# Optimization experiments

Measured on AMD Instinct MI355X. Metric: run time of the kernel, lower is better.

Reference implementation:

```python
import jax, jax.numpy as jnp
import numpy as np

N_NODES = 50000
N_RAND_EDGES = 800000
NEG_SLOPE = 0.2


def setup_inputs() -> dict:
    key = jax.random.key(0)
    ks = jax.random.split(key, 10)
    src_r = jax.random.randint(ks[0], (N_RAND_EDGES,), 0, N_NODES, dtype=jnp.int32)
    dst_r = jax.random.randint(ks[1], (N_RAND_EDGES,), 0, N_NODES, dtype=jnp.int32)
    loops = jnp.arange(N_NODES, dtype=jnp.int32)
    src = jnp.concatenate([src_r, loops])  # [E] with self-loops -> no empty softmax segment
    dst = jnp.concatenate([dst_r, loops])
    return {
        "x": jax.random.normal(ks[2], (N_NODES, 256), dtype=jnp.float32),
        "src": src,
        "dst": dst,
        "W0": jax.random.normal(ks[3], (256, 4 * 64), dtype=jnp.float32) * 0.05,
        "al0": jax.random.normal(ks[4], (4, 64), dtype=jnp.float32) * 0.05,
        "ar0": jax.random.normal(ks[5], (4, 64), dtype=jnp.float32) * 0.05,
        "W1": jax.random.normal(ks[6], (256, 1 * 32), dtype=jnp.float32) * 0.05,
        "al1": jax.random.normal(ks[7], (1, 32), dtype=jnp.float32) * 0.05,
        "ar1": jax.random.normal(ks[8], (1, 32), dtype=jnp.float32) * 0.05,
        "Wres": jax.random.normal(ks[9], (256, 32), dtype=jnp.float32) * 0.05,
    }


def gat_conv(x, src, dst, W, al, ar, Wres, activation):
    """DGL-style GATConv. x: [N, F]; W: [F, H*D]; al/ar: [H, D]."""
    N = x.shape[0]
    H, D = al.shape
    feat = (x @ W).reshape(N, H, D)                       # [N,H,D]
    el = jnp.sum(feat * al, axis=-1)                      # [N,H]
    er = jnp.sum(feat * ar, axis=-1)                      # [N,H]
    e = jax.nn.leaky_relu(el[src] + er[dst], NEG_SLOPE)   # [E,H]
    # edge softmax over incoming edges of each dst node
    emax = jax.ops.segment_max(e, dst, num_segments=N)    # [N,H]
    ex = jnp.exp(e - emax[dst])
    denom = jax.ops.segment_sum(ex, dst, num_segments=N)  # [N,H]
    alpha = ex / denom[dst]                               # [E,H]
    msg = feat[src] * alpha[:, :, None]                   # [E,H,D]
    out = jax.ops.segment_sum(msg, dst, num_segments=N)   # [N,H,D]
    if Wres is not None:
        out = out + (x @ Wres).reshape(N, -1, D)          # residual (broadcast over heads)
    if activation is not None:
        out = activation(out)
    return out


def reference(x, src, dst, W0, al0, ar0, W1, al1, ar1, Wres):
    N = x.shape[0]
    h = gat_conv(x, src, dst, W0, al0, ar0, None, jax.nn.elu)  # [N,4,64]
    h = h.reshape(N, -1)                                       # flatten(1) -> [N,256]
    out = gat_conv(h, src, dst, W1, al1, ar1, Wres, None)      # [N,1,32]
    logits = out.mean(axis=1)                                  # [N,32]
    return logits
```

## Files before the change

### kernel.cpp

```cpp
#include <hip/hip_runtime.h>
#include <math.h>

#define NEG_SLOPE 0.2f

typedef __attribute__((ext_vector_type(8))) short short8;
typedef __attribute__((ext_vector_type(4))) float f32x4;
typedef unsigned int uintx2 __attribute__((ext_vector_type(2)));
typedef unsigned int uintx4 __attribute__((ext_vector_type(4)));

__device__ __forceinline__ float leaky(float x) { return x > 0.f ? x : NEG_SLOPE * x; }
__device__ __forceinline__ unsigned enc(float f) {
    unsigned u = __float_as_uint(f);
    return (u & 0x80000000u) ? ~u : (u | 0x80000000u);
}
__device__ __forceinline__ float dec(unsigned e) {
    return (e & 0x80000000u) ? __uint_as_float(e ^ 0x80000000u) : __uint_as_float(~e);
}
__device__ __forceinline__ unsigned bf16u(float f) {
    unsigned u = __float_as_uint(f);
    return (u + 0x7fffu + ((u >> 16) & 1u)) >> 16;
}
__device__ __forceinline__ float blo(unsigned u) { return __uint_as_float(u << 16); }
__device__ __forceinline__ float bhi(unsigned u) { return __uint_as_float(u & 0xffff0000u); }

__global__ __launch_bounds__(256) void prep_kernel(const float* __restrict__ W0,
                                                   unsigned short* __restrict__ W0P,
                                                   const float* __restrict__ W1,
                                                   const float* __restrict__ Wres,
                                                   unsigned short* __restrict__ Bt1,
                                                   const int* __restrict__ dst,
                                                   int* __restrict__ deg, int E) {
    int b = blockIdx.x, tid = threadIdx.x;
    if (b < 256) {
        int n = b, k = tid;
        W0P[(k >> 5) * 8192 + n * 32 + (k & 31)] = (unsigned short)bf16u(W0[k * 256 + n]);
    } else if (b < 320) {
        int n = b - 256, k = tid;
        float v = (n < 32) ? W1[k * 32 + n] : Wres[k * 32 + (n - 32)];
        Bt1[n * 256 + k] = (unsigned short)bf16u(v);
    } else {
        int e = (b - 320) * 256 + tid;
        if (e < E) atomicAdd(&deg[dst[e]], 1);
    }
}

__global__ __launch_bounds__(256) void gemm0_all(const float* __restrict__ x,
                                                 const unsigned short* __restrict__ W0P,
                                                 unsigned short* __restrict__ featS,
                                                 float* __restrict__ el0, float* __restrict__ er0,
                                                 const float* __restrict__ al,
                                                 const float* __restrict__ ar,
                                                 unsigned* __restrict__ gmax, int M) {
    __shared__ unsigned short As[64 * 40];
    __shared__ unsigned short Bs[256 * 40];
    __shared__ __align__(16) unsigned short tile[64 * 72];
    __shared__ float sEl[4][64], sEr[4][64];
    const int K = 256;
    int tid = threadIdx.x, lane = tid & 63, wv = tid >> 6;
    int m0 = blockIdx.x * 64;
    int wm = (wv >> 1) * 32, wn = (wv & 1) * 32;
    f32x4 acc[4][2][2] = {};
    int arow = tid >> 2, apart = tid & 3;
    bool avalid = (m0 + arow) < M;
    const float* Ap = x + (size_t)min(m0 + arow, M - 1) * K + apart * 8;

    for (int k0 = 0; k0 < K; k0 += 32) {
        float4 a0 = avalid ? *(const float4*)(Ap + k0) : make_float4(0.f, 0.f, 0.f, 0.f);
        float4 a1 = avalid ? *(const float4*)(Ap + k0 + 4) : make_float4(0.f, 0.f, 0.f, 0.f);
        uint4 ap;
        ap.x = bf16u(a0.x) | (bf16u(a0.y) << 16);
        ap.y = bf16u(a0.z) | (bf16u(a0.w) << 16);
        ap.z = bf16u(a1.x) | (bf16u(a1.y) << 16);
        ap.w = bf16u(a1.z) | (bf16u(a1.w) << 16);
        *(uint4*)&As[arow * 40 + apart * 8] = ap;
        const unsigned short* slab = W0P + (k0 >> 5) * 8192;
#pragma unroll
        for (int p = 0; p < 4; ++p) {
            int q = p * 256 + tid;
            uint4 bv = *(const uint4*)(slab + q * 8);
            *(uint4*)&Bs[(q >> 2) * 40 + (q & 3) * 8] = bv;
        }
        __syncthreads();
        short8 af[2];
#pragma unroll
        for (int i = 0; i < 2; ++i)
            af[i] = *(const short8*)&As[(wm + i * 16 + (lane & 15)) * 40 + (lane >> 4) * 8];
#pragma unroll
        for (int y = 0; y < 4; ++y) {
            short8 bf[2];
#pragma unroll
            for (int j = 0; j < 2; ++j)
                bf[j] = *(const short8*)&Bs[(y * 64 + wn + j * 16 + (lane & 15)) * 40 + (lane >> 4) * 8];
#pragma unroll
            for (int i = 0; i < 2; ++i)
#pragma unroll
                for (int j = 0; j < 2; ++j)
                    acc[y][i][j] = __builtin_amdgcn_mfma_f32_16x16x32_bf16(af[i], bf[j], acc[y][i][j], 0, 0, 0);
        }
        __syncthreads();
    }
    size_t N32 = (size_t)M * 32;
    for (int y = 0; y < 4; ++y) {
#pragma unroll
        for (int i = 0; i < 2; ++i)
#pragma unroll
            for (int j = 0; j < 2; ++j)
#pragma unroll
                for (int r = 0; r < 4; ++r)
                    tile[(wm + i * 16 + (lane >> 4) * 4 + r) * 72 + wn + j * 16 + (lane & 15)] =
                        (unsigned short)bf16u(acc[y][i][j][r]);
        __syncthreads();
#pragma unroll
        for (int u = tid; u < 512; u += 256) {
            int ch = u >> 8, node = (u >> 2) & 63, part = u & 3;
            int row = m0 + node;
            if (row < M) {
                uint4 v = *(const uint4*)&tile[node * 72 + ch * 32 + part * 8];
                *(uint4*)&featS[(size_t)(2 * y + ch) * N32 + (size_t)row * 32 + part * 8] = v;
            }
        }
        {
            int row = tid >> 2, qr = tid & 3;
            float pe = 0.f, pr = 0.f;
            for (int k2 = 0; k2 < 16; ++k2) {
                int c = qr * 16 + k2;
                float f = __uint_as_float((unsigned)tile[row * 72 + c] << 16);
                pe += f * al[y * 64 + c];
                pr += f * ar[y * 64 + c];
            }
            pe += __shfl_xor(pe, 1); pe += __shfl_xor(pe, 2);
            pr += __shfl_xor(pr, 1); pr += __shfl_xor(pr, 2);
            if (qr == 0) {
                bool vv = (m0 + row) < M;
                if (vv) {
                    el0[(m0 + row) * 4 + y] = pe;
                    er0[(m0 + row) * 4 + y] = pr;
                }
                sEl[y][row] = vv ? pe : -1e30f;
                sEr[y][row] = vv ? pr : -1e30f;
            }
        }
        __syncthreads();
    }
    {
        float m1 = sEl[wv][lane];
        float m2 = sEr[wv][lane];
#pragma unroll
        for (int o = 1; o <= 32; o <<= 1) {
            m1 = fmaxf(m1, __shfl_xor(m1, o));
            m2 = fmaxf(m2, __shfl_xor(m2, o));
        }
        if (lane == 0) atomicMax(&gmax[wv], enc(m1));
        if (lane == 1) atomicMax(&gmax[4 + wv], enc(m2));
    }
}

__global__ __launch_bounds__(256) void gemm1_fused(const unsigned short* __restrict__ hbS,
                                                   const unsigned short* __restrict__ Bt,
                                                   float* __restrict__ fcat,
                                                   unsigned short* __restrict__ fg16,
                                                   float* __restrict__ el1, float* __restrict__ er1,
                                                   const float* __restrict__ al,
                                                   const float* __restrict__ ar,
                                                   unsigned* __restrict__ gmax, int M) {
    __shared__ unsigned short As[64 * 40];
    __shared__ unsigned short Bs[64 * 40];
    __shared__ __align__(16) float tileF[64 * 68];
    __shared__ float sEl[64], sEr[64];
    const int K = 256;
    int tid = threadIdx.x, lane = tid & 63, wv = tid >> 6;
    int m0 = blockIdx.x * 64;
    int wm = (wv >> 1) * 32, wn = (wv & 1) * 32;
    f32x4 acc[2][2] = {};
    int srow = tid >> 2, scol = (tid & 3) * 8;
    bool avalid = (m0 + srow) < M;
    size_t arow = (size_t)min(m0 + srow, M - 1);
    size_t N32 = (size_t)M * 32;
    const unsigned short* Bp = Bt + (size_t)srow * K + scol;

    for (int k0 = 0; k0 < K; k0 += 32) {
        const unsigned short* Ap = hbS + (size_t)(k0 >> 5) * N32 + arow * 32 + scol;
        uint4 av = avalid ? *(const uint4*)Ap : make_uint4(0, 0, 0, 0);
        float4 bv = *(const float4*)(Bp + k0);
        *(uint4*)&As[srow * 40 + scol] = av;
        *(float4*)&Bs[srow * 40 + scol] = bv;
        __syncthreads();
        short8 af[2], bf[2];
#pragma unroll
        for (int i = 0; i < 2; ++i) {
            af[i] = *(const short8*)&As[(wm + i * 16 + (lane & 15)) * 40 + (lane >> 4) * 8];
            bf[i] = *(const short8*)&Bs[(wn + i * 16 + (lane & 15)) * 40 + (lane >> 4) * 8];
        }
#pragma unroll
        for (int i = 0; i < 2; ++i)
#pragma unroll
            for (int j = 0; j < 2; ++j)
                acc[i][j] = __builtin_amdgcn_mfma_f32_16x16x32_bf16(af[i], bf[j], acc[i][j], 0, 0, 0);
        __syncthreads();
    }
#pragma unroll
    for (int i = 0; i < 2; ++i)
#pragma unroll
        for (int j = 0; j < 2; ++j)
#pragma unroll
            for (int r = 0; r < 4; ++r)
                tileF[(wm + i * 16 + (lane >> 4) * 4 + r) * 68 + wn + j * 16 + (lane & 15)] =
                    acc[i][j][r];
    __syncthreads();
#pragma unroll
    for (int u = tid; u < 1024; u += 256) {
        int node = u >> 4, part = u & 15;
        int row = m0 + node;
        if (row < M)
            *(uint4*)&fcat[(size_t)row * 64 + part * 4] = *(const uint4*)&tileF[node * 68 + part * 4];
    }
#pragma unroll
    for (int u = tid; u < 1024; u += 256) {
        int node = u >> 4, part = u & 15;
        int row = m0 + node;
        if (row < M) {
            float f0 = tileF[node * 68 + part * 2];
            float f1 = tileF[node * 68 + part * 2 + 1];
            ((unsigned*)fg16)[(size_t)row * 16 + part] = bf16u(f0) | (bf16u(f1) << 16);
        }
    }
    {
        int row = tid >> 2, qr = tid & 3;
        float pe = 0.f, pr = 0.f;
        for (int k = 0; k < 8; ++k) {
            int c = qr * 8 + k;
            float f = tileF[row * 68 + c];
            pe += f * al[c];
            pr += f * ar[c];
        }
        pe += __shfl_xor(pe, 1); pe += __shfl_xor(pe, 2);
        pr += __shfl_xor(pr, 1); pr += __shfl_xor(pr, 2);
        if (qr == 0) {
            bool vv = (m0 + row) < M;
            if (vv) {
                el1[m0 + row] = pe;
                er1[m0 + row] = pr;
            }
            sEl[row] = vv ? pe : -1e30f;
            sEr[row] = vv ? pr : -1e30f;
        }
    }
    __syncthreads();
    if (tid < 64) {
        float m = sEl[tid];
#pragma unroll
        for (int o = 1; o <= 32; o <<= 1) m = fmaxf(m, __shfl_xor(m, o));
        if (tid == 0) atomicMax(&gmax[8], enc(m));
    } else if (tid < 128) {
        float m = sEr[tid - 64];
#pragma unroll
        for (int o = 1; o <= 32; o <<= 1) m = fmaxf(m, __shfl_xor(m, o));
        if (tid == 64) atomicMax(&gmax[9], enc(m));
    }
}

__global__ __launch_bounds__(256) void scanA(const int* __restrict__ deg, int* __restrict__ bsum, int N) {
    int i = blockIdx.x * 256 + threadIdx.x;
    int v = (i < N) ? deg[i] : 0;
#pragma unroll
    for (int o = 32; o > 0; o >>= 1) v += __shfl_xor(v, o);
    __shared__ int s[4];
    if ((threadIdx.x & 63) == 0) s[threadIdx.x >> 6] = v;
    __syncthreads();
    if (threadIdx.x == 0) bsum[blockIdx.x] = s[0] + s[1] + s[2] + s[3];
}

__global__ __launch_bounds__(256) void scanB(const int* __restrict__ bsum, int* __restrict__ bpre, int nb) {
    __shared__ int s[256];
    int t = threadIdx.x;
    int v = (t < nb) ? bsum[t] : 0;
    s[t] = v;
    __syncthreads();
    for (int o = 1; o < 256; o <<= 1) {
        int x = (t >= o) ? s[t - o] : 0;
        __syncthreads();
        s[t] += x;
        __syncthreads();
    }
    if (t < nb) bpre[t] = s[t] - v;
}

__global__ __launch_bounds__(256) void scanC(const int* __restrict__ deg, const int* __restrict__ bpre,
                                             int* __restrict__ off, int N) {
    int b = blockIdx.x, t = threadIdx.x;
    int i = b * 256 + t;
    int v = (i < N) ? deg[i] : 0;
    __shared__ int s[256];
    s[t] = v;
    __syncthreads();
    for (int o = 1; o < 256; o <<= 1) {
        int x = (t >= o) ? s[t - o] : 0;
        __syncthreads();
        s[t] += x;
        __syncthreads();
    }
    int incl = s[t];
    int base = bpre[b];
    if (i < N) off[i] = base + incl - v;
    if (i == N - 1) off[N] = base + incl;
}

__global__ void scatter_kernel(const int* __restrict__ src, const int* __restrict__ dst,
                               const int* __restrict__ off, int* __restrict__ cursor,
                               int* __restrict__ csr_src, int E) {
    int e = blockIdx.x * 256 + threadIdx.x;
    if (e < E) {
        int d = dst[e];
        int pos = atomicAdd(&cursor[d], 1);
        csr_src[off[d] + pos] = src[e];
    }
}

__global__ __launch_bounds__(256) void w0norm(const float* __restrict__ el,
                                              const float* __restrict__ er,
                                              const unsigned* __restrict__ gmax,
                                              const int* __restrict__ off,
                                              const int* __restrict__ csr_src,
                                              unsigned* __restrict__ pk0,
                                              float* __restrict__ dinv0, int N, int E) {
    int tid = threadIdx.x, lane = tid & 63, wv = tid >> 6;
    int grp = lane >> 4, j = lane & 15;
    float C0 = leaky(dec(gmax[0]) + dec(gmax[4]));
    float C1 = leaky(dec(gmax[1]) + dec(gmax[5]));
    float C2 = leaky(dec(gmax[2]) + dec(gmax[6]));
    float C3 = leaky(dec(gmax[3]) + dec(gmax[7]));
    int n = blockIdx.x * 16 + wv * 4 + grp;
    if (n >= N) return;
    int base = off[n], deg = off[n + 1] - base;
    float4 ern = *(const float4*)&er[n * 4];
    float d0 = 0.f, d1 = 0.f, d2 = 0.f, d3 = 0.f;
    for (int j0 = 0; j0 < deg; j0 += 16) {
        int jj = j0 + j;
        if (jj < deg) {
            int idx = base + jj;
            int s = csr_src[idx];
            float4 e4 = *(const float4*)&el[s * 4];
            unsigned b0 = bf16u(__expf(leaky(e4.x + ern.x) - C0));
            unsigned b1 = bf16u(__expf(leaky(e4.y + ern.y) - C1));
            unsigned b2 = bf16u(__expf(leaky(e4.z + ern.z) - C2));
            unsigned b3 = bf16u(__expf(leaky(e4.w + ern.w) - C3));
            unsigned sh = (unsigned)s << 16;
            pk0[idx] = sh | b0;
            pk0[E + idx] = sh | b1;
            pk0[2 * E + idx] = sh | b2;
            pk0[3 * E + idx] = sh | b3;
            d0 += __uint_as_float(b0 << 16);
            d1 += __uint_as_float(b1 << 16);
            d2 += __uint_as_float(b2 << 16);
            d3 += __uint_as_float(b3 << 16);
        }
    }
#pragma unroll
    for (int o = 1; o <= 8; o <<= 1) {
        d0 += __shfl_xor(d0, o);
        d1 += __shfl_xor(d1, o);
        d2 += __shfl_xor(d2, o);
        d3 += __shfl_xor(d3, o);
    }
    if (j == 0) {
        float4 iv = make_float4(1.f / d0, 1.f / d1, 1.f / d2, 1.f / d3);
        *(float4*)&dinv0[n * 4] = iv;
    }
}

__global__ __launch_bounds__(256) void w1norm(const float* __restrict__ el,
                                              const float* __restrict__ er,
                                              const unsigned* __restrict__ gmax,
                                              const int* __restrict__ off,
                                              const int* __restrict__ csr_src,
                                              unsigned* __restrict__ pk1,
                                              float* __restrict__ dinv1, int N) {
    int tid = threadIdx.x, lane = tid & 63, wv = tid >> 6;
    float C = leaky(dec(gmax[8]) + dec(gmax[9]));
    int n = blockIdx.x * 4 + wv;
    if (n >= N) return;
    int base = off[n], deg = off[n + 1] - base;
    float ern = er[n];
    float den = 0.f;
    for (int j0 = 0; j0 < deg; j0 += 64) {
        int jj = j0 + lane;
        if (jj < deg) {
            int idx = base + jj;
            int s = csr_src[idx];
            unsigned b = bf16u(__expf(leaky(el[s] + ern) - C));
            pk1[idx] = ((unsigned)s << 16) | b;
            den += __uint_as_float(b << 16);
        }
    }
#pragma unroll
    for (int o = 1; o <= 32; o <<= 1) den += __shfl_xor(den, o);
    if (lane == 0) dinv1[n] = 1.f / den;
}

__global__ __launch_bounds__(256) void agg0_kernel(const unsigned short* __restrict__ featS,
                                                   const unsigned* __restrict__ pk0,
                                                   const float* __restrict__ dinv0,
                                                   const int* __restrict__ off,
                                                   unsigned short* __restrict__ hbS, int N, int E) {
    int tid = threadIdx.x;
    int c = blockIdx.x & 7, h = c >> 1;
    int gblk = blockIdx.x >> 3, G = gridDim.x >> 3;
    int grp = tid >> 2, ld = tid & 3;
    size_t N32 = (size_t)N * 32;
    const char* Fb = (const char*)(featS + (size_t)c * N32) + ld * 16;
    const unsigned* PH = pk0 + (size_t)h * E;
    for (int n = gblk * 64 + grp; n < N; n += G * 64) {
        int base = off[n], deg = off[n + 1] - base;
        float a0 = 0.f, a1 = 0.f, a2 = 0.f, a3 = 0.f;
        float a4 = 0.f, a5 = 0.f, a6 = 0.f, a7 = 0.f;
        const unsigned* P = PH + base;
        int j = 0;
        for (; j + 4 <= deg; j += 4) {
            unsigned p0 = P[j], p1 = P[j + 1], p2 = P[j + 2], p3 = P[j + 3];
            uintx4 u0 = *(const uintx4*)(Fb + (size_t)(p0 >> 16) * 64);
            uintx4 u1 = *(const uintx4*)(Fb + (size_t)(p1 >> 16) * 64);
            uintx4 u2 = *(const uintx4*)(Fb + (size_t)(p2 >> 16) * 64);
            uintx4 u3 = *(const uintx4*)(Fb + (size_t)(p3 >> 16) * 64);
            float w0 = blo(p0), w1 = blo(p1), w2 = blo(p2), w3 = blo(p3);
            a0 += w0 * blo(u0.x); a1 += w0 * bhi(u0.x);
            a2 += w0 * blo(u0.y); a3 += w0 * bhi(u0.y);
            a4 += w0 * blo(u0.z); a5 += w0 * bhi(u0.z);
            a6 += w0 * blo(u0.w); a7 += w0 * bhi(u0.w);
            a0 += w1 * blo(u1.x); a1 += w1 * bhi(u1.x);
            a2 += w1 * blo(u1.y); a3 += w1 * bhi(u1.y);
            a4 += w1 * blo(u1.z); a5 += w1 * bhi(u1.z);
            a6 += w1 * blo(u1.w); a7 += w1 * bhi(u1.w);
            a0 += w2 * blo(u2.x); a1 += w2 * bhi(u2.x);
            a2 += w2 * blo(u2.y); a3 += w2 * bhi(u2.y);
            a4 += w2 * blo(u2.z); a5 += w2 * bhi(u2.z);
            a6 += w2 * blo(u2.w); a7 += w2 * bhi(u2.w);
            a0 += w3 * blo(u3.x); a1 += w3 * bhi(u3.x);
            a2 += w3 * blo(u3.y); a3 += w3 * bhi(u3.y);
            a4 += w3 * blo(u3.z); a5 += w3 * bhi(u3.z);
            a6 += w3 * blo(u3.w); a7 += w3 * bhi(u3.w);
        }
        for (; j < deg; ++j) {
            unsigned p = P[j];
            float w = blo(p);
            uintx4 u = *(const uintx4*)(Fb + (size_t)(p >> 16) * 64);
            a0 += w * blo(u.x); a1 += w * bhi(u.x);
            a2 += w * blo(u.y); a3 += w * bhi(u.y);
            a4 += w * blo(u.z); a5 += w * bhi(u.z);
            a6 += w * blo(u.w); a7 += w * bhi(u.w);
        }
        float inv = dinv0[n * 4 + h];
        float v0 = a0 * inv, v1 = a1 * inv, v2 = a2 * inv, v3 = a3 * inv;
        float v4 = a4 * inv, v5 = a5 * inv, v6 = a6 * inv, v7 = a7 * inv;
        v0 = v0 > 0.f ? v0 : (__expf(v0) - 1.f);
        v1 = v1 > 0.f ? v1 : (__expf(v1) - 1.f);
        v2 = v2 > 0.f ? v2 : (__expf(v2) - 1.f);
        v3 = v3 > 0.f ? v3 : (__expf(v3) - 1.f);
        v4 = v4 > 0.f ? v4 : (__expf(v4) - 1.f);
        v5 = v5 > 0.f ? v5 : (__expf(v5) - 1.f);
        v6 = v6 > 0.f ? v6 : (__expf(v6) - 1.f);
        v7 = v7 > 0.f ? v7 : (__expf(v7) - 1.f);
        uintx4 o;
        o.x = bf16u(v0) | (bf16u(v1) << 16);
        o.y = bf16u(v2) | (bf16u(v3) << 16);
        o.z = bf16u(v4) | (bf16u(v5) << 16);
        o.w = bf16u(v6) | (bf16u(v7) << 16);
        __builtin_nontemporal_store(o, (uintx4*)&hbS[(size_t)c * N32 + (size_t)n * 32 + ld * 8]);
    }
}

__global__ __launch_bounds__(256) void agg1_kernel(const float* __restrict__ fcat,
                                                   const unsigned short* __restrict__ fg16,
                                                   const unsigned* __restrict__ pk1,
                                                   const float* __restrict__ dinv1,
                                                   const int* __restrict__ off,
                                                   float* __restrict__ out, int N) {
    int tid = threadIdx.x;
    int grp = tid >> 3, ld = tid & 7;
    const char* Fb = (const char*)fg16 + ld * 8;
    for (int n = blockIdx.x * 32 + grp; n < N; n += gridDim.x * 32) {
        int base = off[n], deg = off[n + 1] - base;
        float a0 = 0.f, a1 = 0.f, a2 = 0.f, a3 = 0.f;
        const unsigned* P = pk1 + base;
        int j = 0;
        for (; j + 4 <= deg; j += 4) {
            unsigned p0 = P[j], p1 = P[j + 1], p2 = P[j + 2], p3 = P[j + 3];
            uintx2 u0 = *(const uintx2*)(Fb + (size_t)(p0 >> 16) * 64);
            uintx2 u1 = *(const uintx2*)(Fb + (size_t)(p1 >> 16) * 64);
            uintx2 u2 = *(const uintx2*)(Fb + (size_t)(p2 >> 16) * 64);
            uintx2 u3 = *(const uintx2*)(Fb + (size_t)(p3 >> 16) * 64);
            float w0 = blo(p0), w1 = blo(p1), w2 = blo(p2), w3 = blo(p3);
            a0 += w0 * blo(u0.x); a1 += w0 * bhi(u0.x);
            a2 += w0 * blo(u0.y); a3 += w0 * bhi(u0.y);
            a0 += w1 * blo(u1.x); a1 += w1 * bhi(u1.x);
            a2 += w1 * blo(u1.y); a3 += w1 * bhi(u1.y);
            a0 += w2 * blo(u2.x); a1 += w2 * bhi(u2.x);
            a2 += w2 * blo(u2.y); a3 += w2 * bhi(u2.y);
            a0 += w3 * blo(u3.x); a1 += w3 * bhi(u3.x);
            a2 += w3 * blo(u3.y); a3 += w3 * bhi(u3.y);
        }
        for (; j < deg; ++j) {
            unsigned p = P[j];
            float w = blo(p);
            uintx2 u = *(const uintx2*)(Fb + (size_t)(p >> 16) * 64);
            a0 += w * blo(u.x); a1 += w * bhi(u.x);
            a2 += w * blo(u.y); a3 += w * bhi(u.y);
        }
        float inv = dinv1[n];
        f32x4 res = *(const f32x4*)&fcat[(size_t)n * 64 + 32 + ld * 4];
        f32x4 o;
        o.x = a0 * inv + res.x;
        o.y = a1 * inv + res.y;
        o.z = a2 * inv + res.z;
        o.w = a3 * inv + res.w;
        __builtin_nontemporal_store(o, (f32x4*)&out[(size_t)n * 32 + ld * 4]);
    }
}

extern "C" void kernel_launch(void* const* d_in, const int* in_sizes, int n_in,
                              void* d_out, int out_size, void* d_ws, size_t ws_size,
                              hipStream_t stream) {
    const float* x    = (const float*)d_in[0];
    const int*   src  = (const int*)d_in[1];
    const int*   dst  = (const int*)d_in[2];
    const float* W0   = (const float*)d_in[3];
    const float* al0  = (const float*)d_in[4];
    const float* ar0  = (const float*)d_in[5];
    const float* W1   = (const float*)d_in[6];
    const float* al1  = (const float*)d_in[7];
    const float* ar1  = (const float*)d_in[8];
    const float* Wres = (const float*)d_in[9];
    float* out = (float*)d_out;

    const int N = in_sizes[0] / 256;
    const int E = in_sizes[1];

    unsigned short* hbS   = (unsigned short*)d_ws;
    unsigned short* featS = hbS + (size_t)N * 256;
    unsigned short* W0P   = featS + (size_t)N * 256;
    unsigned short* Bt1   = W0P + 256 * 256;
    unsigned short* fg16  = Bt1 + 64 * 256;
    float* fcat  = (float*)(fg16 + (size_t)N * 32);
    float* el0   = fcat + (size_t)N * 64;
    float* er0   = el0 + (size_t)N * 4;
    float* el1   = er0 + (size_t)N * 4;
    float* er1   = el1 + N;
    float* dinv0 = er1 + N;
    float* dinv1 = dinv0 + (size_t)N * 4;
    unsigned* pk0 = (unsigned*)(dinv1 + N);
    unsigned* pk1 = pk0 + (size_t)E * 4;
    int*   deg    = (int*)(pk1 + E);
    int*   cursor = deg + N;
    unsigned* gmax = (unsigned*)(cursor + N);
    int*   offs  = (int*)(gmax + 16);
    int*   bsum  = offs + N + 1;
    int*   bpre  = bsum + 256;
    int*   csr_src = bpre + 256;

    const int nb = (N + 255) / 256;
    const int eb = (E + 255) / 256;
    const int mb = (N + 63) / 64;

    hipMemsetAsync(deg, 0, (size_t)(2 * N + 16) * sizeof(int), stream);

    prep_kernel<<<320 + eb, 256, 0, stream>>>(W0, W0P, W1, Wres, Bt1, dst, deg, E);

    scanA<<<nb, 256, 0, stream>>>(deg, bsum, N);
    scanB<<<1, 256, 0, stream>>>(bsum, bpre, nb);
    scanC<<<nb, 256, 0, stream>>>(deg, bpre, offs, N);
    scatter_kernel<<<eb, 256, 0, stream>>>(src, dst, offs, cursor, csr_src, E);

    gemm0_all<<<mb, 256, 0, stream>>>(x, W0P, featS, el0, er0, al0, ar0, gmax, N);
    w0norm<<<(N + 15) / 16, 256, 0, stream>>>(el0, er0, gmax, offs, csr_src, pk0, dinv0, N, E);
    {
        int G = (N + 63) / 64;
        agg0_kernel<<<G * 8, 256, 0, stream>>>(featS, pk0, dinv0, offs, hbS, N, E);
    }

    gemm1_fused<<<mb, 256, 0, stream>>>(hbS, Bt1, fcat, fg16, el1, er1, al1, ar1, gmax, N);
    w1norm<<<(N + 3) / 4, 256, 0, stream>>>(el1, er1, gmax, offs, csr_src, pk1, dinv1, N);
    {
        int G = (N + 31) / 32;
        agg1_kernel<<<G, 256, 0, stream>>>(fcat, fg16, pk1, dinv1, offs, out, N);
    }
}
```

Baseline: 270.7 us.

## Prefetch next K-slab into registers and compute attention logits from accumulators

Result: slower. 331.9 us (+22.6%).

```diff
diff --git a/kernel.cpp b/kernel.cpp
--- a/kernel.cpp
+++ b/kernel.cpp
@@ -53,8 +53,9 @@
                                                  unsigned* __restrict__ gmax, int M) {
     __shared__ unsigned short As[64 * 40];
     __shared__ unsigned short Bs[256 * 40];
-    __shared__ __align__(16) unsigned short tile[64 * 72];
-    __shared__ float sEl[4][64], sEr[4][64];
+    __shared__ float sAl[256], sAr[256];
+    __shared__ float sElP[2][64], sErP[2][64];
+    unsigned short* tile = Bs;
     const int K = 256;
     int tid = threadIdx.x, lane = tid & 63, wv = tid >> 6;
     int m0 = blockIdx.x * 64;
@@ -63,24 +64,37 @@
     int arow = tid >> 2, apart = tid & 3;
     bool avalid = (m0 + arow) < M;
     const float* Ap = x + (size_t)min(m0 + arow, M - 1) * K + apart * 8;
+    const float4 z4 = make_float4(0.f, 0.f, 0.f, 0.f);
+
+    sAl[tid] = al[tid];
+    sAr[tid] = ar[tid];
+
+    float4 a0 = avalid ? *(const float4*)Ap : z4;
+    float4 a1 = avalid ? *(const float4*)(Ap + 4) : z4;
+    uint4 b[4];
+#pragma unroll
+    for (int p = 0; p < 4; ++p) b[p] = *(const uint4*)(W0P + (p * 256 + tid) * 8);
 
     for (int k0 = 0; k0 < K; k0 += 32) {
-        float4 a0 = avalid ? *(const float4*)(Ap + k0) : make_float4(0.f, 0.f, 0.f, 0.f);
-        float4 a1 = avalid ? *(const float4*)(Ap + k0 + 4) : make_float4(0.f, 0.f, 0.f, 0.f);
         uint4 ap;
         ap.x = bf16u(a0.x) | (bf16u(a0.y) << 16);
         ap.y = bf16u(a0.z) | (bf16u(a0.w) << 16);
         ap.z = bf16u(a1.x) | (bf16u(a1.y) << 16);
         ap.w = bf16u(a1.z) | (bf16u(a1.w) << 16);
         *(uint4*)&As[arow * 40 + apart * 8] = ap;
-        const unsigned short* slab = W0P + (k0 >> 5) * 8192;
 #pragma unroll
         for (int p = 0; p < 4; ++p) {
             int q = p * 256 + tid;
-            uint4 bv = *(const uint4*)(slab + q * 8);
-            *(uint4*)&Bs[(q >> 2) * 40 + (q & 3) * 8] = bv;
-        }
-        __syncthreads();
+            *(uint4*)&Bs[(q >> 2) * 40 + (q & 3) * 8] = b[p];
+        }
+        __syncthreads();
+        if (k0 + 32 < K) {
+            a0 = avalid ? *(const float4*)(Ap + k0 + 32) : z4;
+            a1 = avalid ? *(const float4*)(Ap + k0 + 36) : z4;
+            const unsigned short* slab = W0P + ((k0 >> 5) + 1) * 8192;
+#pragma unroll
+            for (int p = 0; p < 4; ++p) b[p] = *(const uint4*)(slab + (p * 256 + tid) * 8);
+        }
         short8 af[2];
 #pragma unroll
         for (int i = 0; i < 2; ++i)
@@ -95,20 +109,47 @@
             for (int i = 0; i < 2; ++i)
 #pragma unroll
                 for (int j = 0; j < 2; ++j)
-                    acc[y][i][j] = __builtin_amdgcn_mfma_f32_16x16x32_bf16(af[i], bf[j], acc[y][i][j], 0, 0, 0);
-        }
-        __syncthreads();
-    }
+                    acc[y][i][j] = __builtin_amdgcn_mfma_f32_16x16x32_bf16(bf[j], af[i], acc[y][i][j], 0, 0, 0);
+        }
+        __syncthreads();
+    }
+
     size_t N32 = (size_t)M * 32;
     for (int y = 0; y < 4; ++y) {
 #pragma unroll
         for (int i = 0; i < 2; ++i)
 #pragma unroll
-            for (int j = 0; j < 2; ++j)
-#pragma unroll
-                for (int r = 0; r < 4; ++r)
-                    tile[(wm + i * 16 + (lane >> 4) * 4 + r) * 72 + wn + j * 16 + (lane & 15)] =
-                        (unsigned short)bf16u(acc[y][i][j][r]);
+            for (int j = 0; j < 2; ++j) {
+                int node = wm + i * 16 + (lane & 15);
+                int c0 = wn + j * 16 + (lane >> 4) * 4;
+                uint2 pk;
+                pk.x = bf16u(acc[y][i][j][0]) | (bf16u(acc[y][i][j][1]) << 16);
+                pk.y = bf16u(acc[y][i][j][2]) | (bf16u(acc[y][i][j][3]) << 16);
+                *(uint2*)&tile[node * 72 + c0] = pk;
+            }
+        float pe0 = 0.f, pe1 = 0.f, pr0 = 0.f, pr1 = 0.f;
+#pragma unroll
+        for (int j = 0; j < 2; ++j)
+#pragma unroll
+            for (int r = 0; r < 4; ++r) {
+                int c = wn + j * 16 + (lane >> 4) * 4 + r;
+                float av = sAl[y * 64 + c], rv = sAr[y * 64 + c];
+                pe0 += acc[y][0][j][r] * av;
+                pe1 += acc[y][1][j][r] * av;
+                pr0 += acc[y][0][j][r] * rv;
+                pr1 += acc[y][1][j][r] * rv;
+            }
+        pe0 += __shfl_xor(pe0, 16); pe0 += __shfl_xor(pe0, 32);
+        pe1 += __shfl_xor(pe1, 16); pe1 += __shfl_xor(pe1, 32);
+        pr0 += __shfl_xor(pr0, 16); pr0 += __shfl_xor(pr0, 32);
+        pr1 += __shfl_xor(pr1, 16); pr1 += __shfl_xor(pr1, 32);
+        {
+            int g = lane >> 4;
+            float v = (g == 0) ? pe0 : (g == 1) ? pe1 : (g == 2) ? pr0 : pr1;
+            int node = wm + (g & 1) * 16 + (lane & 15);
+            if (g < 2) sElP[wv & 1][node] = v;
+            else       sErP[wv & 1][node] = v;
+        }
         __syncthreads();
 #pragma unroll
         for (int u = tid; u < 512; u += 256) {
@@ -120,38 +161,23 @@
             }
         }
         {
-            int row = tid >> 2, qr = tid & 3;
-            float pe = 0.f, pr = 0.f;
-            for (int k2 = 0; k2 < 16; ++k2) {
-                int c = qr * 16 + k2;
-                float f = __uint_as_float((unsigned)tile[row * 72 + c] << 16);
-                pe += f * al[y * 64 + c];
-                pr += f * ar[y * 64 + c];
+            float mval = -1e30f;
+            if (tid < 128) {
+                int node = tid & 63;
+                bool isEl = tid < 64;
+                float v = isEl ? (sElP[0][node] + sElP[1][node]) : (sErP[0][node] + sErP[1][node]);
+                if (m0 + node < M) {
+                    if (isEl) el0[(m0 + node) * 4 + y] = v;
+                    else      er0[(m0 + node) * 4 + y] = v;
+                    mval = v;
+                }
             }
-            pe += __shfl_xor(pe, 1); pe += __shfl_xor(pe, 2);
-            pr += __shfl_xor(pr, 1); pr += __shfl_xor(pr, 2);
-            if (qr == 0) {
-                bool vv = (m0 + row) < M;
-                if (vv) {
-                    el0[(m0 + row) * 4 + y] = pe;
-                    er0[(m0 + row) * 4 + y] = pr;
-                }
-                sEl[y][row] = vv ? pe : -1e30f;
-                sEr[y][row] = vv ? pr : -1e30f;
-            }
-        }
-        __syncthreads();
-    }
-    {
-        float m1 = sEl[wv][lane];
-        float m2 = sEr[wv][lane];
-#pragma unroll
-        for (int o = 1; o <= 32; o <<= 1) {
-            m1 = fmaxf(m1, __shfl_xor(m1, o));
-            m2 = fmaxf(m2, __shfl_xor(m2, o));
-        }
-        if (lane == 0) atomicMax(&gmax[wv], enc(m1));
-        if (lane == 1) atomicMax(&gmax[4 + wv], enc(m2));
+#pragma unroll
+            for (int o = 1; o <= 32; o <<= 1) mval = fmaxf(mval, __shfl_xor(mval, o));
+            if (tid == 0) atomicMax(&gmax[y], enc(mval));
+            if (tid == 64) atomicMax(&gmax[4 + y], enc(mval));
+        }
+        __syncthreads();
     }
 }
 
@@ -166,7 +192,7 @@
     __shared__ unsigned short As[64 * 40];
     __shared__ unsigned short Bs[64 * 40];
     __shared__ __align__(16) float tileF[64 * 68];
-    __shared__ float sEl[64], sEr[64];
+    __shared__ float sAl1[32], sAr1[32], sEl[64], sEr[64];
     const int K = 256;
     int tid = threadIdx.x, lane = tid & 63, wv = tid >> 6;
     int m0 = blockIdx.x * 64;
@@ -178,13 +204,23 @@
     size_t N32 = (size_t)M * 32;
     const unsigned short* Bp = Bt + (size_t)srow * K + scol;
 
+    if (tid < 32) {
+        sAl1[tid] = al[tid];
+        sAr1[tid] = ar[tid];
+    }
+
+    uint4 areg = avalid ? *(const uint4*)(hbS + arow * 32 + scol) : make_uint4(0, 0, 0, 0);
+    uint4 breg = *(const uint4*)Bp;
+
     for (int k0 = 0; k0 < K; k0 += 32) {
-        const unsigned short* Ap = hbS + (size_t)(k0 >> 5) * N32 + arow * 32 + scol;
-        uint4 av = avalid ? *(const uint4*)Ap : make_uint4(0, 0, 0, 0);
-        float4 bv = *(const float4*)(Bp + k0);
-        *(uint4*)&As[srow * 40 + scol] = av;
-        *(float4*)&Bs[srow * 40 + scol] = bv;
-        __syncthreads();
+        *(uint4*)&As[srow * 40 + scol] = areg;
+        *(uint4*)&Bs[srow * 40 + scol] = breg;
+        __syncthreads();
+        if (k0 + 32 < K) {
+            areg = avalid ? *(const uint4*)(hbS + (size_t)((k0 >> 5) + 1) * N32 + arow * 32 + scol)
+                          : make_uint4(0, 0, 0, 0);
+            breg = *(const uint4*)(Bp + k0 + 32);
+        }
         short8 af[2], bf[2];
 #pragma unroll
         for (int i = 0; i < 2; ++i) {
@@ -195,17 +231,41 @@
         for (int i = 0; i < 2; ++i)
 #pragma unroll
             for (int j = 0; j < 2; ++j)
-                acc[i][j] = __builtin_amdgcn_mfma_f32_16x16x32_bf16(af[i], bf[j], acc[i][j], 0, 0, 0);
-        __syncthreads();
-    }
+                acc[i][j] = __builtin_amdgcn_mfma_f32_16x16x32_bf16(bf[j], af[i], acc[i][j], 0, 0, 0);
+        __syncthreads();
+    }
+
 #pragma unroll
     for (int i = 0; i < 2; ++i)
 #pragma unroll
+        for (int j = 0; j < 2; ++j) {
+            int node = wm + i * 16 + (lane & 15);
+            int c0 = wn + j * 16 + (lane >> 4) * 4;
+            *(f32x4*)&tileF[node * 68 + c0] = acc[i][j];
+        }
+    if ((wv & 1) == 0) {
+        float pe0 = 0.f, pe1 = 0.f, pr0 = 0.f, pr1 = 0.f;
+#pragma unroll
         for (int j = 0; j < 2; ++j)
 #pragma unroll
-            for (int r = 0; r < 4; ++r)
-                tileF[(wm + i * 16 + (lane >> 4) * 4 + r) * 68 + wn + j * 16 + (lane & 15)] =
-                    acc[i][j][r];
+            for (int r = 0; r < 4; ++r) {
+                int c = j * 16 + (lane >> 4) * 4 + r;
+                float av = sAl1[c], rv = sAr1[c];
+                pe0 += acc[0][j][r] * av;
+                pe1 += acc[1][j][r] * av;
+                pr0 += acc[0][j][r] * rv;
+                pr1 += acc[1][j][r] * rv;
+            }
+        pe0 += __shfl_xor(pe0, 16); pe0 += __shfl_xor(pe0, 32);
+        pe1 += __shfl_xor(pe1, 16); pe1 += __shfl_xor(pe1, 32);
+        pr0 += __shfl_xor(pr0, 16); pr0 += __shfl_xor(pr0, 32);
+        pr1 += __shfl_xor(pr1, 16); pr1 += __shfl_xor(pr1, 32);
+        int g = lane >> 4;
+        float v = (g == 0) ? pe0 : (g == 1) ? pe1 : (g == 2) ? pr0 : pr1;
+        int node = wm + (g & 1) * 16 + (lane & 15);
+        if (g < 2) sEl[node] = v;
+        else       sEr[node] = v;
+    }
     __syncthreads();
 #pragma unroll
     for (int u = tid; u < 1024; u += 256) {
@@ -225,37 +285,21 @@
         }
     }
     {
-        int row = tid >> 2, qr = tid & 3;
-        float pe = 0.f, pr = 0.f;
-        for (int k = 0; k < 8; ++k) {
-            int c = qr * 8 + k;
-            float f = tileF[row * 68 + c];
-            pe += f * al[c];
-            pr += f * ar[c];
-        }
-        pe += __shfl_xor(pe, 1); pe += __shfl_xor(pe, 2);
-        pr += __shfl_xor(pr, 1); pr += __shfl_xor(pr, 2);
-        if (qr == 0) {
-            bool vv = (m0 + row) < M;
-            if (vv) {
-                el1[m0 + row] = pe;
-                er1[m0 + row] = pr;
+        float mval = -1e30f;
+        if (tid < 128) {
+            int node = tid & 63;
+            bool isEl = tid < 64;
+            float v = isEl ? sEl[node] : sEr[node];
+            if (m0 + node < M) {
+                if (isEl) el1[m0 + node] = v;
+                else      er1[m0 + node] = v;
+                mval = v;
             }
-            sEl[row] = vv ? pe : -1e30f;
-            sEr[row] = vv ? pr : -1e30f;
-        }
-    }
-    __syncthreads();
-    if (tid < 64) {
-        float m = sEl[tid];
-#pragma unroll
-        for (int o = 1; o <= 32; o <<= 1) m = fmaxf(m, __shfl_xor(m, o));
-        if (tid == 0) atomicMax(&gmax[8], enc(m));
-    } else if (tid < 128) {
-        float m = sEr[tid - 64];
-#pragma unroll
-        for (int o = 1; o <= 32; o <<= 1) m = fmaxf(m, __shfl_xor(m, o));
-        if (tid == 64) atomicMax(&gmax[9], enc(m));
+        }
+#pragma unroll
+        for (int o = 1; o <= 32; o <<= 1) mval = fmaxf(mval, __shfl_xor(mval, o));
+        if (tid == 0) atomicMax(&gmax[8], enc(mval));
+        if (tid == 64) atomicMax(&gmax[9], enc(mval));
     }
 }
 
```
